# Kernel optimization log

Hardware: AMD Instinct MI355X
Metric: run time of the kernel (lower is better)

Reference implementation:

```python
import jax, jax.numpy as jnp
import numpy as np

TEMPERATURE = 0.07
TOP_MARGIN = 0.95
BOTTOM_MARGIN = 0.05

BATCH = 8192
DIM = 1024


def setup_inputs() -> dict:
    key = jax.random.key(0)
    kA, kB = jax.random.split(key)
    embedding_A = jax.random.normal(kA, (BATCH, DIM), dtype=jnp.float32)
    embedding_B = jax.random.normal(kB, (BATCH, DIM), dtype=jnp.float32)
    return {"embedding_A": embedding_A, "embedding_B": embedding_B}


def _l2norm(x):
    return x * jax.lax.rsqrt(jnp.sum(x * x, axis=-1, keepdims=True))


def reference(embedding_A, embedding_B):
    a = _l2norm(embedding_A)
    b = _l2norm(embedding_B)
    B = a.shape[0]
    sim = a @ b.T                                   # [B, B]
    pos = jnp.diagonal(sim)                         # [B]
    eye = jnp.eye(B, dtype=bool)
    upper = pos[:, None] * TOP_MARGIN
    lower = pos[:, None] * BOTTOM_MARGIN
    neg_mask = (sim <= upper) & (sim >= lower) & ~eye   # [B, B]

    # Per-row CE over [positive, hard negatives] == masked logsumexp - pos/tau.
    z = sim / TEMPERATURE
    full_mask = neg_mask | eye                      # positive always included
    masked = jnp.where(full_mask, z, -jnp.inf)
    m = jnp.max(masked, axis=1, keepdims=True)      # finite: diag always present
    lse = m[:, 0] + jnp.log(jnp.sum(jnp.exp(masked - m), axis=1))
    per_row = lse - pos / TEMPERATURE               # [B]

    valid = jnp.any(neg_mask, axis=1)               # rows with >=1 negative
    count = jnp.sum(valid)
    total = jnp.sum(jnp.where(valid, per_row, 0.0))
    return total / jnp.maximum(count, 1).astype(total.dtype)
```

## Files before the change

kernel.cpp:

```cpp
#include <hip/hip_runtime.h>
#include <hip/hip_bf16.h>

#define BATCH 8192
#define DIM   1024
#define INV_TAU (1.0f / 0.07f)
#define TOPM 0.95f
#define BOTM 0.05f

#define BM 256
#define BN 256
#define BK 64
#define NT (DIM / BK)

typedef __attribute__((ext_vector_type(4))) float f32x4;
typedef __attribute__((ext_vector_type(8))) short bf16x8;

typedef __attribute__((address_space(3))) void       lds_void_t;
typedef const __attribute__((address_space(1))) void gbl_void_t;

__device__ inline void async_copy16(const void* g, void* l) {
    __builtin_amdgcn_global_load_lds((gbl_void_t*)g, (lds_void_t*)l, 16, 0, 0);
}

__device__ inline unsigned short f2bf(float f) {
    __hip_bfloat16 h = __float2bfloat16(f);
    return *reinterpret_cast<unsigned short*>(&h);
}

__global__ __launch_bounds__(256) void prep_kernel(
    const float* __restrict__ A, const float* __restrict__ B,
    unsigned short* __restrict__ An, unsigned short* __restrict__ Bn,
    float* __restrict__ pos, float* __restrict__ S)
{
    int row = blockIdx.x;
    int t = threadIdx.x;
    const float4* a4 = (const float4*)(A + (size_t)row * DIM);
    const float4* b4 = (const float4*)(B + (size_t)row * DIM);
    float4 av = a4[t];
    float4 bv = b4[t];
    float sa = av.x*av.x + av.y*av.y + av.z*av.z + av.w*av.w;
    float sb = bv.x*bv.x + bv.y*bv.y + bv.z*bv.z + bv.w*bv.w;
    float dp = av.x*bv.x + av.y*bv.y + av.z*bv.z + av.w*bv.w;
    #pragma unroll
    for (int d = 32; d > 0; d >>= 1) {
        sa += __shfl_down(sa, d);
        sb += __shfl_down(sb, d);
        dp += __shfl_down(dp, d);
    }
    __shared__ float red[3][4];
    int lane = t & 63, w = t >> 6;
    if (lane == 0) { red[0][w] = sa; red[1][w] = sb; red[2][w] = dp; }
    __syncthreads();
    sa = red[0][0] + red[0][1] + red[0][2] + red[0][3];
    sb = red[1][0] + red[1][1] + red[1][2] + red[1][3];
    dp = red[2][0] + red[2][1] + red[2][2] + red[2][3];
    float ra = rsqrtf(sa);
    float rb = rsqrtf(sb);
    if (t == 0) {
        pos[row] = dp * ra * rb;
        S[row] = 0.0f;
    }
    ushort4 oa, ob;
    oa.x = f2bf(av.x * ra); oa.y = f2bf(av.y * ra);
    oa.z = f2bf(av.z * ra); oa.w = f2bf(av.w * ra);
    ob.x = f2bf(bv.x * rb); ob.y = f2bf(bv.y * rb);
    ob.z = f2bf(bv.z * rb); ob.w = f2bf(bv.w * rb);
    ((ushort4*)(An + (size_t)row * DIM))[t] = oa;
    ((ushort4*)(Bn + (size_t)row * DIM))[t] = ob;
}

__global__ __launch_bounds__(512, 2) void sim_loss_kernel(
    const unsigned short* __restrict__ An, const unsigned short* __restrict__ Bn,
    const float* __restrict__ pos, float* __restrict__ S)
{
    __shared__ char lds[131072];

    int tid  = threadIdx.x;
    int lane = tid & 63;
    int wave = tid >> 6;
    int wm = wave >> 2, wn = wave & 3;
    int fr = lane & 15;
    int q  = lane >> 4;

    int bid = blockIdx.x;

#define BASES(g, rB, cB) do {                                                        \
    int xcd_ = bid & 7, jj_ = bid >> 3;                                              \
    int qr_ = (g) >> 1, qc_ = ((g) & 1) ^ (qr_ & 1);                                 \
    (rB) = (qr_ * 16 + (xcd_ >> 1) * 4 + (jj_ >> 3)) * BM;                           \
    (cB) = (qc_ * 16 + (xcd_ & 1) * 8 + (jj_ & 7)) * BN;                             \
} while (0)

    f32x4 acc[8][4] = {};
    bf16x8 a[4][2];
    bf16x8 b[2][2][2];

    int sw = (fr & 7) << 4;
    int c0 = (q * 16) ^ sw;
    int c1 = (64 + q * 16) ^ sw;
    int aRow = (wm * 128 + fr) * 128;
    int bRow = (wn * 64 + fr) * 128;

    int strow = tid >> 3;
    int scb   = ((tid & 7) * 16) ^ ((strow & 7) << 4);
    int ldst = tid * 16;

#define PANELS(rB, cB, pA, pB) do {                                                  \
    (pA) = (const char*)An + (size_t)((rB) + strow) * 2048 + scb;                    \
    (pB) = (const char*)Bn + (size_t)((cB) + strow) * 2048 + scb;                    \
} while (0)

#define STAGE(gbase, u, h, ldsdst) do {                                              \
    async_copy16((gbase) + (size_t)(h) * 262144 + (size_t)(u) * 128,                 \
                 (ldsdst) + (h) * 16384 + ldst);                                     \
    async_copy16((gbase) + (size_t)(h) * 262144 + 131072 + (size_t)(u) * 128,        \
                 (ldsdst) + (h) * 16384 + 8192 + ldst);                              \
} while (0)

#define LDA(sAp, mh) do {                                                            \
    _Pragma("unroll") for (int m = 0; m < 4; ++m) {                                  \
        a[m][0] = *(const bf16x8*)((sAp) + aRow + (mh) * 8192 + m * 2048 + c0);      \
        a[m][1] = *(const bf16x8*)((sAp) + aRow + (mh) * 8192 + m * 2048 + c1);      \
    }                                                                                \
} while (0)

#define LDB(sBp, nh) do {                                                            \
    _Pragma("unroll") for (int n = 0; n < 2; ++n) {                                  \
        b[nh][n][0] = *(const bf16x8*)((sBp) + bRow + (nh) * 4096 + n * 2048 + c0);  \
        b[nh][n][1] = *(const bf16x8*)((sBp) + bRow + (nh) * 4096 + n * 2048 + c1);  \
    }                                                                                \
} while (0)

#define MM(mh, nh) do {                                                              \
    _Pragma("unroll") for (int m = 0; m < 4; ++m)                                    \
    _Pragma("unroll") for (int n = 0; n < 2; ++n) {                                  \
        acc[(mh)*4+m][(nh)*2+n] = __builtin_amdgcn_mfma_f32_16x16x32_bf16(           \
            a[m][0], b[nh][n][0], acc[(mh)*4+m][(nh)*2+n], 0, 0, 0);                 \
        acc[(mh)*4+m][(nh)*2+n] = __builtin_amdgcn_mfma_f32_16x16x32_bf16(           \
            a[m][1], b[nh][n][1], acc[(mh)*4+m][(nh)*2+n], 0, 0, 0);                 \
    }                                                                                \
} while (0)

#define BAR() __builtin_amdgcn_s_barrier()
#define SCH() __builtin_amdgcn_sched_barrier(0)
#define LGKM(n) do { asm volatile("s_waitcnt lgkmcnt(" #n ")" ::: "memory");         \
                     SCH(); } while (0)
#define VMC(n)  asm volatile("s_waitcnt vmcnt(" #n ")" ::: "memory")
#define PRI1() __builtin_amdgcn_s_setprio(1)
#define PRI0() __builtin_amdgcn_s_setprio(0)

#define KTILE(p, gA_, uA, gB_, uB) do {                                              \
    const char* sAp = lds + (p) * 32768;                                             \
    const char* sBp = lds + 65536 + (p) * 32768;                                     \
    char* stA = lds + ((p) ^ 1) * 32768;                                             \
    char* stB = lds + 65536 + (p) * 32768;                                           \
                             \
    LDA(sAp, 0); LDB(sBp, 0); LDB(sBp, 1); STAGE((gA_), (uA), 0, stA);               \
    LGKM(4); PRI1(); MM(0, 0); PRI0(); BAR();                                        \
                                                                    \
    STAGE((gA_), (uA), 1, stA);                                                      \
    LGKM(0); PRI1(); MM(0, 1); PRI0(); BAR(); SCH();                                 \
                                                               \
    LDA(sAp, 1); STAGE((gB_), (uB), 0, stB);                                         \
    LGKM(0); PRI1(); MM(1, 1); PRI0(); BAR();                                        \
                                     \
    STAGE((gB_), (uB), 1, stB);                                                      \
    PRI1(); MM(1, 0); PRI0(); VMC(4); BAR(); SCH();                                  \
} while (0)

    int rowB, colB;
    BASES(0, rowB, colB);
    const char *gAc, *gBc;
    PANELS(rowB, colB, gAc, gBc);

    STAGE(gAc, 0, 0, lds);
    STAGE(gAc, 0, 1, lds);
    STAGE(gBc, 0, 0, lds + 65536);
    STAGE(gBc, 0, 1, lds + 65536);
    STAGE(gBc, 1, 0, lds + 65536 + 32768);
    STAGE(gBc, 1, 1, lds + 65536 + 32768);
    VMC(4);
    BAR();
    SCH();

    #pragma unroll 1
    for (int g = 0; g < 4; ++g) {
        int gn = (g < 3) ? g + 1 : 3;
        int rowBn, colBn;
        BASES(gn, rowBn, colBn);
        const char *gAn2, *gBn2;
        PANELS(rowBn, colBn, gAn2, gBn2);

        #pragma unroll 1
        for (int tt = 0; tt < 7; ++tt) {
            KTILE(0, gAc, 2 * tt + 1, gBc, 2 * tt + 2);
            KTILE(1, gAc, 2 * tt + 2, gBc, 2 * tt + 3);
        }
        KTILE(0, gAc, 15, gBn2, 0);
        KTILE(1, gAn2, 0, gBn2, 1);

        #pragma unroll
        for (int m = 0; m < 8; ++m) {
            #pragma unroll
            for (int j2 = 0; j2 < 4; ++j2) {
                int i = rowB + wm * 128 + m * 16 + q * 4 + j2;
                float p  = pos[i];
                float up = TOPM * p, lo = BOTM * p;
                float rs = 0.0f;
                #pragma unroll
                for (int n = 0; n < 4; ++n) {
                    float sv = acc[m][n][j2];
                    int col = colB + wn * 64 + n * 16 + fr;
                    if (sv <= up && sv >= lo && col != i)
                        rs += __expf((sv - p) * INV_TAU);
                }
                #pragma unroll
                for (int d = 1; d < 16; d <<= 1)
                    rs += __shfl_xor(rs, d);
                if (fr == 0 && rs != 0.0f)
                    atomicAdd(&S[i], rs);
            }
        }
        #pragma unroll
        for (int m2 = 0; m2 < 8; ++m2)
            #pragma unroll
            for (int n2 = 0; n2 < 4; ++n2)
                acc[m2][n2] = (f32x4){0.0f, 0.0f, 0.0f, 0.0f};

        gAc = gAn2; gBc = gBn2; rowB = rowBn; colB = colBn;
    }
    VMC(0);

#undef BASES
#undef PANELS
#undef STAGE
#undef LDA
#undef LDB
#undef MM
#undef BAR
#undef SCH
#undef LGKM
#undef VMC
#undef PRI1
#undef PRI0
#undef KTILE
}

__global__ __launch_bounds__(256) void finalize_kernel(
    const float* __restrict__ S, float* __restrict__ out)
{
    int t = threadIdx.x;
    float tot = 0.0f;
    int c = 0;
    for (int i = t; i < BATCH; i += 256) {
        float s = S[i];
        if (s > 0.0f) { tot += log1pf(s); c += 1; }
    }
    #pragma unroll
    for (int d = 32; d > 0; d >>= 1) {
        tot += __shfl_down(tot, d);
        c   += __shfl_down(c, d);
    }
    __shared__ float st[4];
    __shared__ int   sc[4];
    int lane = t & 63, w = t >> 6;
    if (lane == 0) { st[w] = tot; sc[w] = c; }
    __syncthreads();
    if (t == 0) {
        float T = st[0] + st[1] + st[2] + st[3];
        int   C = sc[0] + sc[1] + sc[2] + sc[3];
        out[0] = T / (float)(C > 0 ? C : 1);
    }
}

extern "C" void kernel_launch(void* const* d_in, const int* in_sizes, int n_in,
                              void* d_out, int out_size, void* d_ws, size_t ws_size,
                              hipStream_t stream) {
    const float* A = (const float*)d_in[0];
    const float* B = (const float*)d_in[1];

    char* ws = (char*)d_ws;
    unsigned short* An = (unsigned short*)ws;
    unsigned short* Bn = An + (size_t)BATCH * DIM;
    float* pos = (float*)(Bn + (size_t)BATCH * DIM);
    float* S   = pos + BATCH;
    float* out = (float*)d_out;

    prep_kernel<<<BATCH, 256, 0, stream>>>(A, B, An, Bn, pos, S);
    sim_loss_kernel<<<256, 512, 0, stream>>>(An, Bn, pos, S);
    finalize_kernel<<<1, 256, 0, stream>>>(S, out);
}
```

Baseline: 202.6 us.

## Software-pipeline LDS fragment loads across k-tiles with ping-pong register buffers

```diff
diff --git a/kernel.cpp b/kernel.cpp
--- a/kernel.cpp
+++ b/kernel.cpp
@@ -92,8 +92,10 @@
 } while (0)
 
     f32x4 acc[8][4] = {};
-    bf16x8 a[4][2];
-    bf16x8 b[2][2][2];
+    bf16x8 A0[4][2];
+    bf16x8 A1[4][2];
+    bf16x8 Bx[2][2];
+    bf16x8 By[2][2];
 
     int sw = (fr & 7) << 4;
     int c0 = (q * 16) ^ sw;
@@ -117,27 +119,29 @@
                  (ldsdst) + (h) * 16384 + 8192 + ldst);                              \
 } while (0)
 
-#define LDA(sAp, mh) do {                                                            \
+#define LDA_(arr, p, mh) do {                                                        \
+    const char* _s = lds + (p) * 32768;                                              \
     _Pragma("unroll") for (int m = 0; m < 4; ++m) {                                  \
-        a[m][0] = *(const bf16x8*)((sAp) + aRow + (mh) * 8192 + m * 2048 + c0);      \
-        a[m][1] = *(const bf16x8*)((sAp) + aRow + (mh) * 8192 + m * 2048 + c1);      \
+        arr[m][0] = *(const bf16x8*)(_s + aRow + (mh) * 8192 + m * 2048 + c0);       \
+        arr[m][1] = *(const bf16x8*)(_s + aRow + (mh) * 8192 + m * 2048 + c1);       \
     }                                                                                \
 } while (0)
 
-#define LDB(sBp, nh) do {                                                            \
+#define LDB_(arr, p, nh) do {                                                        \
+    const char* _s = lds + 65536 + (p) * 32768;                                      \
     _Pragma("unroll") for (int n = 0; n < 2; ++n) {                                  \
-        b[nh][n][0] = *(const bf16x8*)((sBp) + bRow + (nh) * 4096 + n * 2048 + c0);  \
-        b[nh][n][1] = *(const bf16x8*)((sBp) + bRow + (nh) * 4096 + n * 2048 + c1);  \
+        arr[n][0] = *(const bf16x8*)(_s + bRow + (nh) * 4096 + n * 2048 + c0);       \
+        arr[n][1] = *(const bf16x8*)(_s + bRow + (nh) * 4096 + n * 2048 + c1);       \
     }                                                                                \
 } while (0)
 
-#define MM(mh, nh) do {                                                              \
+#define MM_(aarr, barr, mo, no) do {                                                 \
     _Pragma("unroll") for (int m = 0; m < 4; ++m)                                    \
     _Pragma("unroll") for (int n = 0; n < 2; ++n) {                                  \
-        acc[(mh)*4+m][(nh)*2+n] = __builtin_amdgcn_mfma_f32_16x16x32_bf16(           \
-            a[m][0], b[nh][n][0], acc[(mh)*4+m][(nh)*2+n], 0, 0, 0);                 \
-        acc[(mh)*4+m][(nh)*2+n] = __builtin_amdgcn_mfma_f32_16x16x32_bf16(           \
-            a[m][1], b[nh][n][1], acc[(mh)*4+m][(nh)*2+n], 0, 0, 0);                 \
+        acc[(mo)+m][(no)+n] = __builtin_amdgcn_mfma_f32_16x16x32_bf16(               \
+            aarr[m][0], barr[n][0], acc[(mo)+m][(no)+n], 0, 0, 0);                   \
+        acc[(mo)+m][(no)+n] = __builtin_amdgcn_mfma_f32_16x16x32_bf16(               \
+            aarr[m][1], barr[n][1], acc[(mo)+m][(no)+n], 0, 0, 0);                   \
     }                                                                                \
 } while (0)
 
@@ -149,23 +153,19 @@
 #define PRI1() __builtin_amdgcn_s_setprio(1)
 #define PRI0() __builtin_amdgcn_s_setprio(0)
 
-#define KTILE(p, gA_, uA, gB_, uB) do {                                              \
-    const char* sAp = lds + (p) * 32768;                                             \
-    const char* sBp = lds + 65536 + (p) * 32768;                                     \
-    char* stA = lds + ((p) ^ 1) * 32768;                                             \
-    char* stB = lds + 65536 + (p) * 32768;                                           \
-                             \
-    LDA(sAp, 0); LDB(sBp, 0); LDB(sBp, 1); STAGE((gA_), (uA), 0, stA);               \
-    LGKM(4); PRI1(); MM(0, 0); PRI0(); BAR();                                        \
-                                                                    \
-    STAGE((gA_), (uA), 1, stA);                                                      \
-    LGKM(0); PRI1(); MM(0, 1); PRI0(); BAR(); SCH();                                 \
-                                                               \
-    LDA(sAp, 1); STAGE((gB_), (uB), 0, stB);                                         \
-    LGKM(0); PRI1(); MM(1, 1); PRI0(); BAR();                                        \
-                                     \
-    STAGE((gB_), (uB), 1, stB);                                                      \
-    PRI1(); MM(1, 0); PRI0(); VMC(4); BAR(); SCH();                                  \
+#define KTILE(p, B0A, B1A, pA1, u1, pB2, u2, pA2, u3) do {                           \
+    char* stA1 = lds + ((p) ^ 1) * 32768;                                            \
+    char* stB  = lds + 65536 + (p) * 32768;                                          \
+    char* stA2 = lds + (p) * 32768;                                                  \
+     LDB_(B1A, (p), 1); STAGE((pA1), (u1), 1, stA1);                         \
+    LGKM(4); PRI1(); MM_(A0, B0A, 0, 0); PRI0(); SCH(); BAR(); SCH();                \
+     LDA_(A1, (p), 1);                                                       \
+    LGKM(8); PRI1(); MM_(A0, B1A, 0, 2); PRI0(); VMC(0); SCH(); BAR(); SCH();        \
+     LDA_(A0, (p) ^ 1, 0); STAGE((pB2), (u2), 0, stB);                       \
+    LGKM(8); PRI1(); MM_(A1, B1A, 4, 2); PRI0(); SCH(); BAR(); SCH();                \
+     LDB_(B1A, (p) ^ 1, 0); STAGE((pB2), (u2), 1, stB);                      \
+    STAGE((pA2), (u3), 0, stA2);                                                     \
+    PRI1(); MM_(A1, B0A, 4, 0); PRI0(); SCH(); BAR(); SCH();                         \
 } while (0)
 
     int rowB, colB;
@@ -177,11 +177,14 @@
     STAGE(gAc, 0, 1, lds);
     STAGE(gBc, 0, 0, lds + 65536);
     STAGE(gBc, 0, 1, lds + 65536);
-    STAGE(gBc, 1, 0, lds + 65536 + 32768);
-    STAGE(gBc, 1, 1, lds + 65536 + 32768);
-    VMC(4);
+    STAGE(gBc, 1, 0, lds + 98304);
+    STAGE(gBc, 1, 1, lds + 98304);
+    STAGE(gAc, 1, 0, lds + 32768);
+    VMC(6);
     BAR();
     SCH();
+    LDA_(A0, 0, 0);
+    LDB_(Bx, 0, 0);
 
     #pragma unroll 1
     for (int g = 0; g < 4; ++g) {
@@ -193,11 +196,12 @@
 
         #pragma unroll 1
         for (int tt = 0; tt < 7; ++tt) {
-            KTILE(0, gAc, 2 * tt + 1, gBc, 2 * tt + 2);
-            KTILE(1, gAc, 2 * tt + 2, gBc, 2 * tt + 3);
+            int t0 = 2 * tt;
+            KTILE(0, Bx, By, gAc, t0 + 1, gBc, t0 + 2, gAc, t0 + 2);
+            KTILE(1, By, Bx, gAc, t0 + 2, gBc, t0 + 3, gAc, t0 + 3);
         }
-        KTILE(0, gAc, 15, gBn2, 0);
-        KTILE(1, gAn2, 0, gBn2, 1);
+        KTILE(0, Bx, By, gAc, 15, gBn2, 0, gAn2, 0);
+        KTILE(1, By, Bx, gAn2, 0, gBn2, 1, gAn2, 1);
 
         #pragma unroll
         for (int m = 0; m < 8; ++m) {
@@ -229,14 +233,15 @@
 
         gAc = gAn2; gBc = gBn2; rowB = rowBn; colB = colBn;
     }
+    LGKM(0);
     VMC(0);
 
 #undef BASES
 #undef PANELS
 #undef STAGE
-#undef LDA
-#undef LDB
-#undef MM
+#undef LDA_
+#undef LDB_
+#undef MM_
 #undef BAR
 #undef SCH
 #undef LGKM
```

Measured after the change: 260.2 us. 28.5% more time.
